# Kernel tuning notes

Measured on AMD Instinct MI355X. Metric: run time of the kernel, lower is better.

Reference implementation:

```python
import jax, jax.numpy as jnp
import numpy as np

DIM = 1024
HEADS = 16
SEQ = 1024
BATCH = 4
SCALE = (DIM // HEADS) ** -0.5


def setup_inputs() -> dict:
    key = jax.random.key(0)
    ks = jax.random.split(key, 5)
    x = jax.random.normal(ks[0], (BATCH, SEQ, DIM), dtype=jnp.float32)
    # Linear weights stored [in, out]; y = x @ W + b (math-equivalent to torch Linear)
    w_qkv = jax.random.normal(ks[1], (DIM, 3 * DIM), dtype=jnp.float32) * (DIM ** -0.5)
    b_qkv = jnp.zeros((3 * DIM,), dtype=jnp.float32)
    w_proj = jax.random.normal(ks[2], (DIM, DIM), dtype=jnp.float32) * (DIM ** -0.5)
    b_proj = jnp.zeros((DIM,), dtype=jnp.float32)
    rel_table = jax.random.normal(ks[3], (2 * SEQ - 1, HEADS), dtype=jnp.float32) * 0.02
    coords = jnp.arange(SEQ)
    rel_index = (coords[:, None] - coords[None, :] + SEQ - 1).astype(jnp.int32)  # [N, N]
    return {"x": x, "w_qkv": w_qkv, "b_qkv": b_qkv, "w_proj": w_proj,
            "b_proj": b_proj, "rel_table": rel_table, "rel_index": rel_index}


def reference(x, w_qkv, b_qkv, w_proj, b_proj, rel_table, rel_index):
    B, N, C = x.shape
    H = HEADS
    hd = C // H
    qkv = (x @ w_qkv + b_qkv).reshape(B, N, 3, H, hd).transpose(2, 0, 3, 1, 4)  # [3,B,H,N,hd]
    q, k, v = qkv[0] * SCALE, qkv[1], qkv[2]
    attn = jnp.einsum('bhqe,bhke->bhqk', q, k)                 # [B,H,N,N]
    bias = rel_table[rel_index]                                 # [N,N,H] gather
    attn = attn + bias.transpose(2, 0, 1)[None]                 # add [1,H,N,N]
    attn = jax.nn.softmax(attn, axis=-1)
    # Faithful to the original einsum 'bnqk,bnqe->bnqe' (contracts k over attn only)
    out = jnp.einsum('bnqk,bnqe->bnqe', attn, v)                # [B,H,N,hd]
    out = out.transpose(0, 2, 1, 3).reshape(B, N, C)
    return out @ w_proj + b_proj
```

## Files before the change

kernel.cpp:

```cpp
#include <hip/hip_runtime.h>


#define DIMC 1024
#define MTOT 4096

__device__ __forceinline__ unsigned short f2bf(float f) {
  unsigned u = __float_as_uint(f);
  u += 0x7FFFu + ((u >> 16) & 1u);
  return (unsigned short)(u >> 16);
}

typedef __attribute__((ext_vector_type(8))) short short8;
typedef __attribute__((ext_vector_type(4))) float floatx4;

__device__ __forceinline__ void async_copy16(const unsigned short* g, unsigned short* l) {
  __builtin_amdgcn_global_load_lds(
      (const __attribute__((address_space(1))) unsigned int*)g,
      (__attribute__((address_space(3))) unsigned int*)l,
      16, 0, 0);
}

__global__ void cast_bf16_kernel(const float* __restrict__ in,
                                 unsigned short* __restrict__ out) {
  int i = (blockIdx.x * 256 + threadIdx.x) * 4;
  float4 f = *(const float4*)(in + i);
  ushort4 o;
  o.x = f2bf(f.x); o.y = f2bf(f.y); o.z = f2bf(f.z); o.w = f2bf(f.w);
  *(ushort4*)(out + i) = o;
}

__global__ void transpose_cast_kernel(const float* __restrict__ in, int stride,
                                      int col0, unsigned short* __restrict__ out) {
  __shared__ float tile[32][33];
  const int t = threadIdx.x;
  const int tx = t & 31, ty = t >> 5;
  const int bx = blockIdx.x, by = blockIdx.y;
#pragma unroll
  for (int r = 0; r < 4; ++r) {
    int kl = ty + r * 8;
    tile[kl][tx] = in[(size_t)(by * 32 + kl) * stride + col0 + bx * 32 + tx];
  }
  __syncthreads();
#pragma unroll
  for (int r = 0; r < 4; ++r) {
    int nl = ty + r * 8;
    out[(size_t)(bx * 32 + nl) * DIMC + by * 32 + tx] = f2bf(tile[tx][nl]);
  }
}

template <bool BF16_OUT>
__global__ __launch_bounds__(256, 2) void gemm_bt_kernel(
    const unsigned short* __restrict__ A,
    const unsigned short* __restrict__ Bt,
    const float* __restrict__ bias,
    void* __restrict__ Cout, int M, int N, int K) {
  __shared__ __align__(16) unsigned short As[64 * 32];
  __shared__ __align__(16) unsigned short Bs[128 * 32];
  const int tid = threadIdx.x;
  const int wv = tid >> 6;
  const int lane = tid & 63;
  const int m0 = blockIdx.y * 64;
  const int n0 = blockIdx.x * 128;

  floatx4 acc[4][2] = {};

  const int arow = tid >> 2;
  const int aoff = (tid & 3) * 8;
  const unsigned short* Ag  = A  + (size_t)(m0 + arow) * K + aoff;
  const unsigned short* Bg0 = Bt + (size_t)(n0 + arow) * K + aoff;
  const unsigned short* Bg1 = Bt + (size_t)(n0 + 64 + arow) * K + aoff;
  unsigned short* AsW  = As + wv * 512;
  unsigned short* BsW0 = Bs + wv * 512;
  unsigned short* BsW1 = Bs + 2048 + wv * 512;

  const int lr = lane & 15;
  const int qr = lane >> 4;

  for (int k0 = 0; k0 < K; k0 += 32) {
    async_copy16(Ag + k0, AsW);
    async_copy16(Bg0 + k0, BsW0);
    async_copy16(Bg1 + k0, BsW1);
    __syncthreads();

    short8 a[4], b[2];
#pragma unroll
    for (int mi = 0; mi < 4; ++mi)
      a[mi] = *(const short8*)(As + (mi * 16 + lr) * 32 + qr * 8);
#pragma unroll
    for (int ni = 0; ni < 2; ++ni)
      b[ni] = *(const short8*)(Bs + (wv * 32 + ni * 16 + lr) * 32 + qr * 8);
#pragma unroll
    for (int mi = 0; mi < 4; ++mi)
#pragma unroll
      for (int ni = 0; ni < 2; ++ni)
        acc[mi][ni] = __builtin_amdgcn_mfma_f32_16x16x32_bf16(a[mi], b[ni],
                                                              acc[mi][ni], 0, 0, 0);
    __syncthreads();
  }

#pragma unroll
  for (int mi = 0; mi < 4; ++mi) {
#pragma unroll
    for (int ni = 0; ni < 2; ++ni) {
      const int col = n0 + wv * 32 + ni * 16 + lr;
      const float bv = bias[col];
#pragma unroll
      for (int r = 0; r < 4; ++r) {
        const int row = m0 + mi * 16 + qr * 4 + r;
        const float val = acc[mi][ni][r] + bv;
        if (BF16_OUT)
          ((unsigned short*)Cout)[(size_t)row * N + col] = f2bf(val);
        else
          ((float*)Cout)[(size_t)row * N + col] = val;
      }
    }
  }
}

extern "C" void kernel_launch(void* const* d_in, const int* in_sizes, int n_in,
                              void* d_out, int out_size, void* d_ws, size_t ws_size,
                              hipStream_t stream) {
  const float* x      = (const float*)d_in[0];
  const float* w_qkv  = (const float*)d_in[1];
  const float* b_qkv  = (const float*)d_in[2];
  const float* w_proj = (const float*)d_in[3];
  const float* b_proj = (const float*)d_in[4];
  float* out = (float*)d_out;

  char* ws = (char*)d_ws;
  unsigned short* xb  = (unsigned short*)(ws);
  unsigned short* WvT = (unsigned short*)(ws + (size_t)(8u << 20));
  unsigned short* WpT = (unsigned short*)(ws + (size_t)(10u << 20));
  unsigned short* vb  = (unsigned short*)(ws + (size_t)(12u << 20));

  cast_bf16_kernel<<<(MTOT * DIMC) / (256 * 4), 256, 0, stream>>>(x, xb);
  transpose_cast_kernel<<<dim3(32, 32), 256, 0, stream>>>(w_qkv, 3 * DIMC, 2 * DIMC, WvT);
  transpose_cast_kernel<<<dim3(32, 32), 256, 0, stream>>>(w_proj, DIMC, 0, WpT);
  gemm_bt_kernel<true><<<dim3(DIMC / 128, MTOT / 64), 256, 0, stream>>>(
      xb, WvT, b_qkv + 2 * DIMC, vb, MTOT, DIMC, DIMC);
  gemm_bt_kernel<false><<<dim3(DIMC / 128, MTOT / 64), 256, 0, stream>>>(
      vb, WpT, b_proj, out, MTOT, DIMC, DIMC);
}
```

Measured before the change: 134.2 us.

## Fold V and output projection weights into one combined matrix, widen GEMM K-tile

Since the attention output reduces to v, the V projection and output projection are folded algebraically. The kernel precomputes Wc = Wv·Wp (a 1024³ GEMM) and a combined bias, then runs one 4096×1024×1024 GEMM over x instead of two. This drops the 4096-row intermediate GEMM and its bf16 round trip, at the cost of a per-call weight-product GEMM. The GEMM kernel also moves to a 64-wide K tile with XOR-swizzled LDS to cut bank conflicts and halve barriers.

```diff
diff --git a/kernel.cpp b/kernel.cpp
--- a/kernel.cpp
+++ b/kernel.cpp
@@ -29,6 +29,17 @@
   *(ushort4*)(out + i) = o;
 }
 
+__global__ void cast_slice_kernel(const float* __restrict__ in, int stride,
+                                  int col0, unsigned short* __restrict__ out) {
+  int i4 = blockIdx.x * 256 + threadIdx.x;
+  int r = i4 >> 8;
+  int c = (i4 & 255) * 4;
+  float4 f = *(const float4*)(in + (size_t)r * stride + col0 + c);
+  ushort4 o;
+  o.x = f2bf(f.x); o.y = f2bf(f.y); o.z = f2bf(f.z); o.w = f2bf(f.w);
+  *(ushort4*)(out + (size_t)r * DIMC + c) = o;
+}
+
 __global__ void transpose_cast_kernel(const float* __restrict__ in, int stride,
                                       int col0, unsigned short* __restrict__ out) {
   __shared__ float tile[32][33];
@@ -48,14 +59,30 @@
   }
 }
 
+__global__ void bias_combine_kernel(const float* __restrict__ b_v,
+                                    const float* __restrict__ w_proj,
+                                    const float* __restrict__ b_proj,
+                                    float* __restrict__ b_c) {
+  __shared__ float red[256];
+  const int t = threadIdx.x;
+  const int n = blockIdx.x * 64 + (t & 63);
+  const int q = t >> 6;
+  float s = 0.f;
+  for (int j = q * 256; j < q * 256 + 256; ++j)
+    s += b_v[j] * w_proj[(size_t)j * DIMC + n];
+  red[t] = s;
+  __syncthreads();
+  if (q == 0) b_c[n] = red[t] + red[t + 64] + red[t + 128] + red[t + 192] + b_proj[n];
+}
+
 template <bool BF16_OUT>
 __global__ __launch_bounds__(256, 2) void gemm_bt_kernel(
     const unsigned short* __restrict__ A,
     const unsigned short* __restrict__ Bt,
     const float* __restrict__ bias,
     void* __restrict__ Cout, int M, int N, int K) {
-  __shared__ __align__(16) unsigned short As[64 * 32];
-  __shared__ __align__(16) unsigned short Bs[128 * 32];
+  __shared__ __align__(16) unsigned short As[64 * 64];
+  __shared__ __align__(16) unsigned short Bs[128 * 64];
   const int tid = threadIdx.x;
   const int wv = tid >> 6;
   const int lane = tid & 63;
@@ -64,37 +91,53 @@
 
   floatx4 acc[4][2] = {};
 
-  const int arow = tid >> 2;
-  const int aoff = (tid & 3) * 8;
-  const unsigned short* Ag  = A  + (size_t)(m0 + arow) * K + aoff;
-  const unsigned short* Bg0 = Bt + (size_t)(n0 + arow) * K + aoff;
-  const unsigned short* Bg1 = Bt + (size_t)(n0 + 64 + arow) * K + aoff;
-  unsigned short* AsW  = As + wv * 512;
-  unsigned short* BsW0 = Bs + wv * 512;
-  unsigned short* BsW1 = Bs + 2048 + wv * 512;
+  const int srow = tid >> 3;
+  const int skc = (tid & 7) ^ (srow & 7);
+  const unsigned short* Ag0 = A + (size_t)(m0 + srow) * K + skc * 8;
+  const unsigned short* Ag1 = A + (size_t)(m0 + 32 + srow) * K + skc * 8;
+  const unsigned short* Bg0 = Bt + (size_t)(n0 + srow) * K + skc * 8;
+  const unsigned short* Bg1 = Bt + (size_t)(n0 + 32 + srow) * K + skc * 8;
+  const unsigned short* Bg2 = Bt + (size_t)(n0 + 64 + srow) * K + skc * 8;
+  const unsigned short* Bg3 = Bt + (size_t)(n0 + 96 + srow) * K + skc * 8;
+  unsigned short* AsW0 = As + (0 * 256 + wv * 64) * 8;
+  unsigned short* AsW1 = As + (1 * 256 + wv * 64) * 8;
+  unsigned short* BsW0 = Bs + (0 * 256 + wv * 64) * 8;
+  unsigned short* BsW1 = Bs + (1 * 256 + wv * 64) * 8;
+  unsigned short* BsW2 = Bs + (2 * 256 + wv * 64) * 8;
+  unsigned short* BsW3 = Bs + (3 * 256 + wv * 64) * 8;
 
   const int lr = lane & 15;
   const int qr = lane >> 4;
+  const int lx = lr & 7;
 
-  for (int k0 = 0; k0 < K; k0 += 32) {
-    async_copy16(Ag + k0, AsW);
+  for (int k0 = 0; k0 < K; k0 += 64) {
+    async_copy16(Ag0 + k0, AsW0);
+    async_copy16(Ag1 + k0, AsW1);
     async_copy16(Bg0 + k0, BsW0);
     async_copy16(Bg1 + k0, BsW1);
+    async_copy16(Bg2 + k0, BsW2);
+    async_copy16(Bg3 + k0, BsW3);
     __syncthreads();
 
-    short8 a[4], b[2];
+    short8 a[2][4], b[2][2];
 #pragma unroll
-    for (int mi = 0; mi < 4; ++mi)
-      a[mi] = *(const short8*)(As + (mi * 16 + lr) * 32 + qr * 8);
+    for (int s = 0; s < 2; ++s) {
+      const int kphys = ((s * 4 + qr) ^ lx) * 8;
 #pragma unroll
-    for (int ni = 0; ni < 2; ++ni)
-      b[ni] = *(const short8*)(Bs + (wv * 32 + ni * 16 + lr) * 32 + qr * 8);
-#pragma unroll
-    for (int mi = 0; mi < 4; ++mi)
+      for (int mi = 0; mi < 4; ++mi)
+        a[s][mi] = *(const short8*)(As + (mi * 16 + lr) * 64 + kphys);
 #pragma unroll
       for (int ni = 0; ni < 2; ++ni)
-        acc[mi][ni] = __builtin_amdgcn_mfma_f32_16x16x32_bf16(a[mi], b[ni],
-                                                              acc[mi][ni], 0, 0, 0);
+        b[s][ni] = *(const short8*)(Bs + (wv * 32 + ni * 16 + lr) * 64 + kphys);
+    }
+#pragma unroll
+    for (int s = 0; s < 2; ++s)
+#pragma unroll
+      for (int mi = 0; mi < 4; ++mi)
+#pragma unroll
+        for (int ni = 0; ni < 2; ++ni)
+          acc[mi][ni] = __builtin_amdgcn_mfma_f32_16x16x32_bf16(a[s][mi], b[s][ni],
+                                                                acc[mi][ni], 0, 0, 0);
     __syncthreads();
   }
 
@@ -103,7 +146,7 @@
 #pragma unroll
     for (int ni = 0; ni < 2; ++ni) {
       const int col = n0 + wv * 32 + ni * 16 + lr;
-      const float bv = bias[col];
+      const float bv = bias ? bias[col] : 0.0f;
 #pragma unroll
       for (int r = 0; r < 4; ++r) {
         const int row = m0 + mi * 16 + qr * 4 + r;
@@ -129,15 +172,17 @@
 
   char* ws = (char*)d_ws;
   unsigned short* xb  = (unsigned short*)(ws);
-  unsigned short* WvT = (unsigned short*)(ws + (size_t)(8u << 20));
-  unsigned short* WpT = (unsigned short*)(ws + (size_t)(10u << 20));
-  unsigned short* vb  = (unsigned short*)(ws + (size_t)(12u << 20));
+  unsigned short* WpT = (unsigned short*)(ws + (size_t)(8u << 20));
+  unsigned short* Wvb = (unsigned short*)(ws + (size_t)(10u << 20));
+  unsigned short* WcT = (unsigned short*)(ws + (size_t)(12u << 20));
+  float*          b_c = (float*)(ws + (size_t)(14u << 20));
 
   cast_bf16_kernel<<<(MTOT * DIMC) / (256 * 4), 256, 0, stream>>>(x, xb);
-  transpose_cast_kernel<<<dim3(32, 32), 256, 0, stream>>>(w_qkv, 3 * DIMC, 2 * DIMC, WvT);
   transpose_cast_kernel<<<dim3(32, 32), 256, 0, stream>>>(w_proj, DIMC, 0, WpT);
-  gemm_bt_kernel<true><<<dim3(DIMC / 128, MTOT / 64), 256, 0, stream>>>(
-      xb, WvT, b_qkv + 2 * DIMC, vb, MTOT, DIMC, DIMC);
+  cast_slice_kernel<<<(DIMC * DIMC) / (256 * 4), 256, 0, stream>>>(w_qkv, 3 * DIMC, 2 * DIMC, Wvb);
+  bias_combine_kernel<<<DIMC / 64, 256, 0, stream>>>(b_qkv + 2 * DIMC, w_proj, b_proj, b_c);
+  gemm_bt_kernel<true><<<dim3(DIMC / 128, DIMC / 64), 256, 0, stream>>>(
+      WpT, Wvb, nullptr, WcT, DIMC, DIMC, DIMC);
   gemm_bt_kernel<false><<<dim3(DIMC / 128, MTOT / 64), 256, 0, stream>>>(
-      vb, WpT, b_proj, out, MTOT, DIMC, DIMC);
+      xb, WcT, b_c, out, MTOT, DIMC, DIMC);
 }
```

Result: slower. 191.4 us (+42.6%).
